# Kernel tuning notes

Hardware: AMD Instinct MI355X
Metric: run time of the kernel (lower is better)

## Reference

```python
import jax, jax.numpy as jnp
import numpy as np

B, N, D = 8, 4096, 512

def setup_inputs() -> dict:
    key = jax.random.key(0)
    k1, k2, k3 = jax.random.split(key, 3)
    x = jax.random.normal(k1, (B, N, D), dtype=jnp.float32)
    rotation = jax.random.normal(k2, (D, D), dtype=jnp.float32)
    entangle = jax.random.normal(k3, (D, D), dtype=jnp.float32)
    return {"x": x, "rotation": rotation, "entangle": entangle}

def reference(x, rotation, entangle):
    # query/key projections; note: no V projection, V = x
    query = jnp.einsum("bnd,de->bne", x, rotation)
    key = jnp.einsum("bnd,de->bne", x, entangle)
    scale = 1.0 / jnp.sqrt(jnp.asarray(x.shape[-1], dtype=x.dtype))
    scores = jax.nn.softmax(jnp.einsum("bqd,bkd->bqk", query, key) * scale, axis=-1)
    return jnp.einsum("bqk,bkd->bqd", scores, x)
```

## Files before the change

kernel.cpp:

```cpp
#include <hip/hip_runtime.h>

#define BATCH 8
#define SEQ   4096
#define DIM   512

typedef __attribute__((ext_vector_type(8))) short bf16x8;
typedef __attribute__((ext_vector_type(4))) float f32x4;

__device__ __forceinline__ unsigned short f2bf(float f) {
  unsigned int u = __float_as_uint(f);
  unsigned int r = (u + 0x7fffu + ((u >> 16) & 1u)) >> 16;
  return (unsigned short)r;
}
__device__ __forceinline__ float bf2f(unsigned short s) {
  return __uint_as_float(((unsigned int)s) << 16);
}

__global__ __launch_bounds__(256) void wt_split_kernel(
    const float* __restrict__ rot, const float* __restrict__ ent,
    unsigned short* __restrict__ wrh, unsigned short* __restrict__ wrl,
    unsigned short* __restrict__ weh, unsigned short* __restrict__ wel) {
  const float scale = 0.04419417382415922f;
  int g = blockIdx.x * 256 + threadIdx.x;
  for (int idx = g; idx < 512 * 512; idx += 128 * 256) {
    int d = idx >> 9, e = idx & 511;
    size_t o = (size_t)e * 512 + d;
    float v = rot[idx] * scale;
    unsigned short h = f2bf(v);
    wrh[o] = h; wrl[o] = f2bf(v - bf2f(h));
    float v2 = ent[idx];
    unsigned short h2 = f2bf(v2);
    weh[o] = h2; wel[o] = f2bf(v2 - bf2f(h2));
  }
}

__global__ __launch_bounds__(256) void xt_split_kernel(
    const float* __restrict__ X, unsigned short* __restrict__ Th) {
  __shared__ float T[64][65];
  const int b = blockIdx.z, n0 = blockIdx.x * 64, d0 = blockIdx.y * 64;
  const int tid = threadIdx.x;
  for (int idx = tid; idx < 4096; idx += 256) {
    int r = idx >> 6, c = idx & 63;
    T[r][c] = X[((size_t)(b * SEQ + n0 + r)) * DIM + d0 + c];
  }
  __syncthreads();
  for (int idx = tid; idx < 4096; idx += 256) {
    int r = idx >> 6, c = idx & 63;
    size_t o = ((size_t)(b * DIM + d0 + r)) * SEQ + n0 + c;
    Th[o] = f2bf(T[c][r]);
  }
}

__global__ __launch_bounds__(256, 2) void proj_both(
    const float* __restrict__ X,
    const unsigned short* __restrict__ wrh, const unsigned short* __restrict__ wrl,
    const unsigned short* __restrict__ weh, const unsigned short* __restrict__ wel,
    unsigned short* __restrict__ qh, unsigned short* __restrict__ ql,
    unsigned short* __restrict__ kh, unsigned short* __restrict__ kl) {
  const int tid = threadIdx.x;
  const int w = tid >> 6, lane = tid & 63, l15 = lane & 15, quad = lane >> 4;
  const int rowBase = blockIdx.y * 64 + (w & 1) * 32;
  const int colBase = blockIdx.x * 64 + (w >> 1) * 32;
  f32x4 qa[2][2] = {}, ka[2][2] = {};
  const float* xp[2];
  const unsigned short *rh[2], *rl[2], *eh[2], *el[2];
  xp[0] = X + (size_t)(rowBase + l15) * DIM + quad * 8;
  xp[1] = X + (size_t)(rowBase + 16 + l15) * DIM + quad * 8;
#pragma unroll
  for (int ni = 0; ni < 2; ++ni) {
    size_t o = (size_t)(colBase + ni * 16 + l15) * DIM + quad * 8;
    rh[ni] = wrh + o; rl[ni] = wrl + o; eh[ni] = weh + o; el[ni] = wel + o;
  }
  for (int d0 = 0; d0 < DIM; d0 += 32) {
    bf16x8 ah[2], al[2];
#pragma unroll
    for (int mi = 0; mi < 2; ++mi) {
      const float* p = xp[mi] + d0;
#pragma unroll
      for (int e = 0; e < 8; ++e) {
        float v = p[e];
        unsigned short h = f2bf(v);
        ah[mi][e] = (short)h;
        al[mi][e] = (short)f2bf(v - bf2f(h));
      }
    }
#pragma unroll
    for (int ni = 0; ni < 2; ++ni) {
      bf16x8 bh = *(const bf16x8*)(rh[ni] + d0);
      bf16x8 bl = *(const bf16x8*)(rl[ni] + d0);
      bf16x8 ch = *(const bf16x8*)(eh[ni] + d0);
      bf16x8 cl = *(const bf16x8*)(el[ni] + d0);
#pragma unroll
      for (int mi = 0; mi < 2; ++mi) {
        qa[mi][ni] = __builtin_amdgcn_mfma_f32_16x16x32_bf16(ah[mi], bh, qa[mi][ni], 0, 0, 0);
        qa[mi][ni] = __builtin_amdgcn_mfma_f32_16x16x32_bf16(ah[mi], bl, qa[mi][ni], 0, 0, 0);
        qa[mi][ni] = __builtin_amdgcn_mfma_f32_16x16x32_bf16(al[mi], bh, qa[mi][ni], 0, 0, 0);
        ka[mi][ni] = __builtin_amdgcn_mfma_f32_16x16x32_bf16(ah[mi], ch, ka[mi][ni], 0, 0, 0);
        ka[mi][ni] = __builtin_amdgcn_mfma_f32_16x16x32_bf16(ah[mi], cl, ka[mi][ni], 0, 0, 0);
        ka[mi][ni] = __builtin_amdgcn_mfma_f32_16x16x32_bf16(al[mi], ch, ka[mi][ni], 0, 0, 0);
      }
    }
  }
#pragma unroll
  for (int mi = 0; mi < 2; ++mi)
#pragma unroll
    for (int ni = 0; ni < 2; ++ni)
#pragma unroll
      for (int r = 0; r < 4; ++r) {
        int row = rowBase + mi * 16 + quad * 4 + r;
        int col = colBase + ni * 16 + l15;
        size_t o = (size_t)row * DIM + col;
        float v = qa[mi][ni][r];
        unsigned short h = f2bf(v);
        qh[o] = h; ql[o] = f2bf(v - bf2f(h));
        float v2 = ka[mi][ni][r];
        unsigned short h2 = f2bf(v2);
        kh[o] = h2; kl[o] = f2bf(v2 - bf2f(h2));
      }
}

__global__ __launch_bounds__(256, 2) void attn_mfma(
    const unsigned short* __restrict__ Qh, const unsigned short* __restrict__ Ql,
    const unsigned short* __restrict__ Kh, const unsigned short* __restrict__ Kl,
    const unsigned short* __restrict__ Xth, float* __restrict__ out,
    float* __restrict__ Opart, float* __restrict__ Mp, float* __restrict__ Lp) {
  __shared__ short stage[2][4][2048];
  __shared__ unsigned short PsH[64][72];
  __shared__ float red1[64][2], red2[64][2];
  __shared__ float m_s[64], l_s[64], al_s[64];

  const int tid = threadIdx.x;
  const int w = tid >> 6, lane = tid & 63, l15 = lane & 15, quad = lane >> 4;
  const int b = blockIdx.y, q0 = blockIdx.x * 64;
  const int qsp = (w & 1) * 2, ksp = (w >> 1) * 2;
  const int dbase = w * 128;
  const int ktiles = (SEQ / 64) / gridDim.z;
  const int kbase = blockIdx.z * ktiles * 64;

  if (tid < 64) { m_s[tid] = -3.0e38f; l_s[tid] = 0.0f; }
  __syncthreads();

  f32x4 Of[4][8] = {};

  const int sr = lane >> 2, scm = lane & 3;
  const unsigned short* qsrc = ((w & 1) ? Ql : Qh) + (size_t)(b * SEQ + q0) * DIM;
  const unsigned short* ksrcb = ((w & 1) ? Kl : Kh) + (size_t)b * SEQ * DIM;
  const bool isQ = (w < 2);

  for (int t = 0; t < ktiles; ++t) {
    const int k0 = kbase + t * 64;
    const unsigned short* base = isQ ? qsrc : (ksrcb + (size_t)k0 * DIM);

    {
      bf16x8 g[4];
#pragma unroll
      for (int i = 0; i < 4; ++i) {
        int r = i * 16 + sr, clog = scm ^ (r & 3);
        g[i] = *(const bf16x8*)(base + (size_t)r * DIM + clog * 8);
      }
#pragma unroll
      for (int i = 0; i < 4; ++i) {
        int r = i * 16 + sr;
        *(bf16x8*)&stage[0][w][r * 32 + scm * 8] = g[i];
      }
    }
    __syncthreads();

    f32x4 sa[2][2] = {};
    for (int c = 0; c < 16; ++c) {
      const int bsel = c & 1;
      bf16x8 g[4];
      if (c < 15) {
        const int d0 = (c + 1) * 32;
#pragma unroll
        for (int i = 0; i < 4; ++i) {
          int r = i * 16 + sr, clog = scm ^ (r & 3);
          g[i] = *(const bf16x8*)(base + (size_t)r * DIM + d0 + clog * 8);
        }
      }
      const int cq = (quad ^ (l15 & 3)) * 8;
      bf16x8 a0h = *(const bf16x8*)&stage[bsel][0][((qsp + 0) * 16 + l15) * 32 + cq];
      bf16x8 a0l = *(const bf16x8*)&stage[bsel][1][((qsp + 0) * 16 + l15) * 32 + cq];
      bf16x8 a1h = *(const bf16x8*)&stage[bsel][0][((qsp + 1) * 16 + l15) * 32 + cq];
      bf16x8 a1l = *(const bf16x8*)&stage[bsel][1][((qsp + 1) * 16 + l15) * 32 + cq];
      bf16x8 b0h = *(const bf16x8*)&stage[bsel][2][((ksp + 0) * 16 + l15) * 32 + cq];
      bf16x8 b0l = *(const bf16x8*)&stage[bsel][3][((ksp + 0) * 16 + l15) * 32 + cq];
      bf16x8 b1h = *(const bf16x8*)&stage[bsel][2][((ksp + 1) * 16 + l15) * 32 + cq];
      bf16x8 b1l = *(const bf16x8*)&stage[bsel][3][((ksp + 1) * 16 + l15) * 32 + cq];
      sa[0][0] = __builtin_amdgcn_mfma_f32_16x16x32_bf16(a0h, b0h, sa[0][0], 0, 0, 0);
      sa[0][0] = __builtin_amdgcn_mfma_f32_16x16x32_bf16(a0h, b0l, sa[0][0], 0, 0, 0);
      sa[0][0] = __builtin_amdgcn_mfma_f32_16x16x32_bf16(a0l, b0h, sa[0][0], 0, 0, 0);
      sa[0][1] = __builtin_amdgcn_mfma_f32_16x16x32_bf16(a0h, b1h, sa[0][1], 0, 0, 0);
      sa[0][1] = __builtin_amdgcn_mfma_f32_16x16x32_bf16(a0h, b1l, sa[0][1], 0, 0, 0);
      sa[0][1] = __builtin_amdgcn_mfma_f32_16x16x32_bf16(a0l, b1h, sa[0][1], 0, 0, 0);
      sa[1][0] = __builtin_amdgcn_mfma_f32_16x16x32_bf16(a1h, b0h, sa[1][0], 0, 0, 0);
      sa[1][0] = __builtin_amdgcn_mfma_f32_16x16x32_bf16(a1h, b0l, sa[1][0], 0, 0, 0);
      sa[1][0] = __builtin_amdgcn_mfma_f32_16x16x32_bf16(a1l, b0h, sa[1][0], 0, 0, 0);
      sa[1][1] = __builtin_amdgcn_mfma_f32_16x16x32_bf16(a1h, b1h, sa[1][1], 0, 0, 0);
      sa[1][1] = __builtin_amdgcn_mfma_f32_16x16x32_bf16(a1h, b1l, sa[1][1], 0, 0, 0);
      sa[1][1] = __builtin_amdgcn_mfma_f32_16x16x32_bf16(a1l, b1h, sa[1][1], 0, 0, 0);
      if (c < 15) {
#pragma unroll
        for (int i = 0; i < 4; ++i) {
          int r = i * 16 + sr;
          *(bf16x8*)&stage[1 - bsel][w][r * 32 + scm * 8] = g[i];
        }
      }
      __syncthreads();
    }

    float pm[2][4];
#pragma unroll
    for (int qi = 0; qi < 2; ++qi)
#pragma unroll
      for (int r = 0; r < 4; ++r) {
        float v = fmaxf(sa[qi][0][r], sa[qi][1][r]);
#pragma unroll
        for (int off = 1; off < 16; off <<= 1)
          v = fmaxf(v, __shfl_xor(v, off, 64));
        pm[qi][r] = v;
      }
    if (l15 == 0) {
#pragma unroll
      for (int qi = 0; qi < 2; ++qi)
#pragma unroll
        for (int r = 0; r < 4; ++r)
          red1[(qsp + qi) * 16 + quad * 4 + r][w >> 1] = pm[qi][r];
    }
    __syncthreads();
    if (tid < 64) {
      float mo = m_s[tid];
      float mn = fmaxf(mo, fmaxf(red1[tid][0], red1[tid][1]));
      m_s[tid] = mn;
      al_s[tid] = __expf(mo - mn);
    }
    __syncthreads();

#pragma unroll
    for (int qi = 0; qi < 2; ++qi)
#pragma unroll
      for (int r = 0; r < 4; ++r) {
        const int row = (qsp + qi) * 16 + quad * 4 + r;
        const float m = m_s[row];
        float p0 = __expf(sa[qi][0][r] - m);
        float p1 = __expf(sa[qi][1][r] - m);
        PsH[row][ksp * 16 + l15] = f2bf(p0);
        PsH[row][ksp * 16 + 16 + l15] = f2bf(p1);
        float v = p0 + p1;
#pragma unroll
        for (int off = 1; off < 16; off <<= 1)
          v += __shfl_xor(v, off, 64);
        if (l15 == 0) red2[row][w >> 1] = v;
      }
    __syncthreads();
    if (tid < 64) l_s[tid] = l_s[tid] * al_s[tid] + red2[tid][0] + red2[tid][1];

    float alv[4][4];
#pragma unroll
    for (int qt = 0; qt < 4; ++qt)
#pragma unroll
      for (int r = 0; r < 4; ++r)
        alv[qt][r] = al_s[qt * 16 + quad * 4 + r];
#pragma unroll
    for (int qt = 0; qt < 4; ++qt)
#pragma unroll
      for (int nt = 0; nt < 8; ++nt)
#pragma unroll
        for (int r = 0; r < 4; ++r)
          Of[qt][nt][r] *= alv[qt][r];
#pragma unroll
    for (int ks = 0; ks < 2; ++ks) {
      bf16x8 Ph[4];
#pragma unroll
      for (int qt = 0; qt < 4; ++qt)
        Ph[qt] = *(const bf16x8*)&PsH[qt * 16 + l15][ks * 32 + quad * 8];
      bf16x8 xf[8];
#pragma unroll
      for (int nt = 0; nt < 8; ++nt) {
        const size_t xo =
            ((size_t)(b * DIM + dbase + nt * 16 + l15)) * SEQ + k0 + ks * 32 + quad * 8;
        xf[nt] = *(const bf16x8*)(Xth + xo);
      }
#pragma unroll
      for (int nt = 0; nt < 8; ++nt)
#pragma unroll
        for (int qt = 0; qt < 4; ++qt)
          Of[qt][nt] = __builtin_amdgcn_mfma_f32_16x16x32_bf16(Ph[qt], xf[nt], Of[qt][nt], 0, 0, 0);
    }
    __syncthreads();
  }

  if (gridDim.z == 1) {
    float inv[4][4];
#pragma unroll
    for (int qt = 0; qt < 4; ++qt)
#pragma unroll
      for (int r = 0; r < 4; ++r)
        inv[qt][r] = 1.0f / l_s[qt * 16 + quad * 4 + r];
#pragma unroll
    for (int qt = 0; qt < 4; ++qt)
#pragma unroll
      for (int r = 0; r < 4; ++r) {
        const size_t ro = ((size_t)(b * SEQ + q0 + qt * 16 + quad * 4 + r)) * DIM + dbase;
#pragma unroll
        for (int nt = 0; nt < 8; ++nt)
          out[ro + nt * 16 + l15] = Of[qt][nt][r] * inv[qt][r];
      }
  } else {
    const size_t NE = (size_t)BATCH * SEQ * DIM;
    float* Ob = Opart + (size_t)blockIdx.z * NE;
#pragma unroll
    for (int qt = 0; qt < 4; ++qt)
#pragma unroll
      for (int r = 0; r < 4; ++r) {
        const size_t ro = ((size_t)(b * SEQ + q0 + qt * 16 + quad * 4 + r)) * DIM + dbase;
#pragma unroll
        for (int nt = 0; nt < 8; ++nt)
          Ob[ro + nt * 16 + l15] = Of[qt][nt][r];
      }
    if (tid < 64) {
      size_t ri = (size_t)blockIdx.z * (BATCH * SEQ) + (size_t)b * SEQ + q0 + tid;
      Mp[ri] = m_s[tid];
      Lp[ri] = l_s[tid];
    }
  }
}

__global__ __launch_bounds__(256) void merge_kernel(
    const float* __restrict__ Op, const float* __restrict__ Mp,
    const float* __restrict__ Lp, float* __restrict__ out) {
  const size_t NE = (size_t)BATCH * SEQ * DIM;
  const int NR = BATCH * SEQ;
  size_t i4 = (size_t)blockIdx.x * 256 + threadIdx.x;
  size_t e = i4 * 4;
  int row = (int)(e >> 9);
  float m0 = Mp[row], m1 = Mp[NR + row];
  float l0 = Lp[row], l1 = Lp[NR + row];
  float m = fmaxf(m0, m1);
  float a0 = __expf(m0 - m), a1 = __expf(m1 - m);
  float inv = 1.0f / (a0 * l0 + a1 * l1);
  float4 o0 = *(const float4*)(Op + e);
  float4 o1 = *(const float4*)(Op + NE + e);
  float4 r;
  r.x = (a0 * o0.x + a1 * o1.x) * inv;
  r.y = (a0 * o0.y + a1 * o1.y) * inv;
  r.z = (a0 * o0.z + a1 * o1.z) * inv;
  r.w = (a0 * o0.w + a1 * o1.w) * inv;
  *(float4*)(out + e) = r;
}

extern "C" void kernel_launch(void* const* d_in, const int* in_sizes, int n_in,
                              void* d_out, int out_size, void* d_ws,
                              size_t ws_size, hipStream_t stream) {
  const float* x   = (const float*)d_in[0];
  const float* rot = (const float*)d_in[1];
  const float* ent = (const float*)d_in[2];
  float* out = (float*)d_out;

  const size_t NE = (size_t)BATCH * SEQ * DIM;
  unsigned short* qh  = (unsigned short*)d_ws;
  unsigned short* ql  = qh + NE;
  unsigned short* kh  = ql + NE;
  unsigned short* kl  = kh + NE;
  unsigned short* xth = kl + NE;
  unsigned short* wrh = xth + NE;
  unsigned short* wrl = wrh + 262144;
  unsigned short* weh = wrl + 262144;
  unsigned short* wel = weh + 262144;
  float* Opart = (float*)(wel + 262144);
  float* Mp    = Opart + 2 * NE;
  float* Lp    = Mp + 2 * (BATCH * SEQ);

  const size_t need2 =
      (5 * NE + 4 * 262144) * sizeof(unsigned short) +
      (2 * NE + 4 * (size_t)(BATCH * SEQ)) * sizeof(float);
  const int splits = (ws_size >= need2) ? 2 : 1;

  wt_split_kernel<<<128, 256, 0, stream>>>(rot, ent, wrh, wrl, weh, wel);
  xt_split_kernel<<<dim3(SEQ / 64, DIM / 64, BATCH), 256, 0, stream>>>(x, xth);
  proj_both<<<dim3(DIM / 64, BATCH * SEQ / 64), 256, 0, stream>>>(
      x, wrh, wrl, weh, wel, qh, ql, kh, kl);

  attn_mfma<<<dim3(SEQ / 64, BATCH, splits), 256, 0, stream>>>(
      qh, ql, kh, kl, xth, out, Opart, Mp, Lp);
  if (splits == 2) {
    merge_kernel<<<(unsigned)(NE / 1024), 256, 0, stream>>>(Opart, Mp, Lp, out);
  }
}
```

Before: 1.573 ms.

## Pre-split x to bf16 hi/lo and enlarge attention tile to 128 queries

A new kernel splits x into bf16 high/low planes once, so the projection kernel loads them directly instead of converting fp32 per tile. The attention kernel now uses 512-thread blocks covering 128 query rows, with each wave owning 64 output columns. Each K tile and X^T fragment is therefore reused across twice as many queries, and the redundant trailing sync per tile is dropped. The cost is more registers and LDS per block and half as many blocks. The x split buffers reuse the Opart workspace before attention overwrites it.

```diff
diff --git a/kernel.cpp b/kernel.cpp
--- a/kernel.cpp
+++ b/kernel.cpp
@@ -6,6 +6,7 @@
 
 typedef __attribute__((ext_vector_type(8))) short bf16x8;
 typedef __attribute__((ext_vector_type(4))) float f32x4;
+typedef __attribute__((ext_vector_type(4))) unsigned short us16x4;
 
 __device__ __forceinline__ unsigned short f2bf(float f) {
   unsigned int u = __float_as_uint(f);
@@ -34,6 +35,23 @@
   }
 }
 
+__global__ __launch_bounds__(256) void x_split_kernel(
+    const float* __restrict__ X, unsigned short* __restrict__ Xh,
+    unsigned short* __restrict__ Xl) {
+  size_t i = ((size_t)blockIdx.x * 256 + threadIdx.x) * 4;
+  float4 v = *(const float4*)(X + i);
+  us16x4 hh, ll;
+  float vv[4] = {v.x, v.y, v.z, v.w};
+#pragma unroll
+  for (int e = 0; e < 4; ++e) {
+    unsigned short h = f2bf(vv[e]);
+    hh[e] = h;
+    ll[e] = f2bf(vv[e] - bf2f(h));
+  }
+  *(us16x4*)(Xh + i) = hh;
+  *(us16x4*)(Xl + i) = ll;
+}
+
 __global__ __launch_bounds__(256) void xt_split_kernel(
     const float* __restrict__ X, unsigned short* __restrict__ Th) {
   __shared__ float T[64][65];
@@ -52,7 +70,7 @@
 }
 
 __global__ __launch_bounds__(256, 2) void proj_both(
-    const float* __restrict__ X,
+    const unsigned short* __restrict__ Xh, const unsigned short* __restrict__ Xl,
     const unsigned short* __restrict__ wrh, const unsigned short* __restrict__ wrl,
     const unsigned short* __restrict__ weh, const unsigned short* __restrict__ wel,
     unsigned short* __restrict__ qh, unsigned short* __restrict__ ql,
@@ -62,10 +80,10 @@
   const int rowBase = blockIdx.y * 64 + (w & 1) * 32;
   const int colBase = blockIdx.x * 64 + (w >> 1) * 32;
   f32x4 qa[2][2] = {}, ka[2][2] = {};
-  const float* xp[2];
+  size_t xo[2];
   const unsigned short *rh[2], *rl[2], *eh[2], *el[2];
-  xp[0] = X + (size_t)(rowBase + l15) * DIM + quad * 8;
-  xp[1] = X + (size_t)(rowBase + 16 + l15) * DIM + quad * 8;
+  xo[0] = (size_t)(rowBase + l15) * DIM + quad * 8;
+  xo[1] = (size_t)(rowBase + 16 + l15) * DIM + quad * 8;
 #pragma unroll
   for (int ni = 0; ni < 2; ++ni) {
     size_t o = (size_t)(colBase + ni * 16 + l15) * DIM + quad * 8;
@@ -75,14 +93,8 @@
     bf16x8 ah[2], al[2];
 #pragma unroll
     for (int mi = 0; mi < 2; ++mi) {
-      const float* p = xp[mi] + d0;
-#pragma unroll
-      for (int e = 0; e < 8; ++e) {
-        float v = p[e];
-        unsigned short h = f2bf(v);
-        ah[mi][e] = (short)h;
-        al[mi][e] = (short)f2bf(v - bf2f(h));
-      }
+      ah[mi] = *(const bf16x8*)(Xh + xo[mi] + d0);
+      al[mi] = *(const bf16x8*)(Xl + xo[mi] + d0);
     }
 #pragma unroll
     for (int ni = 0; ni < 2; ++ni) {
@@ -119,74 +131,72 @@
       }
 }
 
-__global__ __launch_bounds__(256, 2) void attn_mfma(
+__global__ __launch_bounds__(512, 4) void attn_mfma(
     const unsigned short* __restrict__ Qh, const unsigned short* __restrict__ Ql,
     const unsigned short* __restrict__ Kh, const unsigned short* __restrict__ Kl,
     const unsigned short* __restrict__ Xth, float* __restrict__ out,
     float* __restrict__ Opart, float* __restrict__ Mp, float* __restrict__ Lp) {
-  __shared__ short stage[2][4][2048];
-  __shared__ unsigned short PsH[64][72];
-  __shared__ float red1[64][2], red2[64][2];
-  __shared__ float m_s[64], l_s[64], al_s[64];
+  __shared__ short stage[2][12288];
+  __shared__ unsigned short PsH[128][72];
+  __shared__ float red1[128][2], red2[128][2];
+  __shared__ float m_s[128], l_s[128], al_s[128];
 
   const int tid = threadIdx.x;
   const int w = tid >> 6, lane = tid & 63, l15 = lane & 15, quad = lane >> 4;
-  const int b = blockIdx.y, q0 = blockIdx.x * 64;
-  const int qsp = (w & 1) * 2, ksp = (w >> 1) * 2;
-  const int dbase = w * 128;
+  const int b = blockIdx.y, q0 = blockIdx.x * 128;
+  const int qsp = (w & 3) * 2, ksp = (w >> 2) * 2;
   const int ktiles = (SEQ / 64) / gridDim.z;
   const int kbase = blockIdx.z * ktiles * 64;
 
-  if (tid < 64) { m_s[tid] = -3.0e38f; l_s[tid] = 0.0f; }
+  if (tid < 128) { m_s[tid] = -3.0e38f; l_s[tid] = 0.0f; }
   __syncthreads();
 
-  f32x4 Of[4][8] = {};
+  f32x4 Of[8][4] = {};
 
   const int sr = lane >> 2, scm = lane & 3;
-  const unsigned short* qsrc = ((w & 1) ? Ql : Qh) + (size_t)(b * SEQ + q0) * DIM;
-  const unsigned short* ksrcb = ((w & 1) ? Kl : Kh) + (size_t)b * SEQ * DIM;
-  const bool isQ = (w < 2);
+  const int jblk = scm ^ ((sr >> 1) & 3);
+  const bool isQ = (w < 4);
+  const int rbase = isQ ? (w & 1) * 64 : ((w >> 1) & 1) * 32;
+  const int ninst = isQ ? 4 : 2;
+  const int plane_off = isQ ? ((w >> 1) & 1) * 4096 : 8192 + (w & 1) * 2048;
+  const unsigned short* gQ = (((w >> 1) & 1) ? Ql : Qh) + (size_t)(b * SEQ + q0) * DIM;
+  const unsigned short* gK = ((w & 1) ? Kl : Kh) + (size_t)b * SEQ * DIM;
+  const int pb = (quad ^ ((l15 >> 1) & 3)) * 8;
 
   for (int t = 0; t < ktiles; ++t) {
     const int k0 = kbase + t * 64;
-    const unsigned short* base = isQ ? qsrc : (ksrcb + (size_t)k0 * DIM);
-
-    {
-      bf16x8 g[4];
-#pragma unroll
-      for (int i = 0; i < 4; ++i) {
-        int r = i * 16 + sr, clog = scm ^ (r & 3);
-        g[i] = *(const bf16x8*)(base + (size_t)r * DIM + clog * 8);
-      }
-#pragma unroll
-      for (int i = 0; i < 4; ++i) {
-        int r = i * 16 + sr;
-        *(bf16x8*)&stage[0][w][r * 32 + scm * 8] = g[i];
-      }
-    }
+    const unsigned short* gbase = isQ ? gQ : (gK + (size_t)k0 * DIM);
+
+    bf16x8 g[4];
+#pragma unroll
+    for (int i = 0; i < 4; ++i)
+      if (i < ninst)
+        g[i] = *(const bf16x8*)(gbase + (size_t)(rbase + i * 16 + sr) * DIM + jblk * 8);
+#pragma unroll
+    for (int i = 0; i < 4; ++i)
+      if (i < ninst)
+        *(bf16x8*)&stage[0][plane_off + (rbase + i * 16 + sr) * 32 + scm * 8] = g[i];
     __syncthreads();
 
     f32x4 sa[2][2] = {};
     for (int c = 0; c < 16; ++c) {
       const int bsel = c & 1;
-      bf16x8 g[4];
       if (c < 15) {
         const int d0 = (c + 1) * 32;
 #pragma unroll
-        for (int i = 0; i < 4; ++i) {
-          int r = i * 16 + sr, clog = scm ^ (r & 3);
-          g[i] = *(const bf16x8*)(base + (size_t)r * DIM + d0 + clog * 8);
-        }
-      }
-      const int cq = (quad ^ (l15 & 3)) * 8;
-      bf16x8 a0h = *(const bf16x8*)&stage[bsel][0][((qsp + 0) * 16 + l15) * 32 + cq];
-      bf16x8 a0l = *(const bf16x8*)&stage[bsel][1][((qsp + 0) * 16 + l15) * 32 + cq];
-      bf16x8 a1h = *(const bf16x8*)&stage[bsel][0][((qsp + 1) * 16 + l15) * 32 + cq];
-      bf16x8 a1l = *(const bf16x8*)&stage[bsel][1][((qsp + 1) * 16 + l15) * 32 + cq];
-      bf16x8 b0h = *(const bf16x8*)&stage[bsel][2][((ksp + 0) * 16 + l15) * 32 + cq];
-      bf16x8 b0l = *(const bf16x8*)&stage[bsel][3][((ksp + 0) * 16 + l15) * 32 + cq];
-      bf16x8 b1h = *(const bf16x8*)&stage[bsel][2][((ksp + 1) * 16 + l15) * 32 + cq];
-      bf16x8 b1l = *(const bf16x8*)&stage[bsel][3][((ksp + 1) * 16 + l15) * 32 + cq];
+        for (int i = 0; i < 4; ++i)
+          if (i < ninst)
+            g[i] = *(const bf16x8*)(gbase + (size_t)(rbase + i * 16 + sr) * DIM + d0 + jblk * 8);
+      }
+      const short* st = stage[bsel];
+      bf16x8 a0h = *(const bf16x8*)&st[((qsp + 0) * 16 + l15) * 32 + pb];
+      bf16x8 a1h = *(const bf16x8*)&st[((qsp + 1) * 16 + l15) * 32 + pb];
+      bf16x8 a0l = *(const bf16x8*)&st[4096 + ((qsp + 0) * 16 + l15) * 32 + pb];
+      bf16x8 a1l = *(const bf16x8*)&st[4096 + ((qsp + 1) * 16 + l15) * 32 + pb];
+      bf16x8 b0h = *(const bf16x8*)&st[8192 + ((ksp + 0) * 16 + l15) * 32 + pb];
+      bf16x8 b1h = *(const bf16x8*)&st[8192 + ((ksp + 1) * 16 + l15) * 32 + pb];
+      bf16x8 b0l = *(const bf16x8*)&st[10240 + ((ksp + 0) * 16 + l15) * 32 + pb];
+      bf16x8 b1l = *(const bf16x8*)&st[10240 + ((ksp + 1) * 16 + l15) * 32 + pb];
       sa[0][0] = __builtin_amdgcn_mfma_f32_16x16x32_bf16(a0h, b0h, sa[0][0], 0, 0, 0);
       sa[0][0] = __builtin_amdgcn_mfma_f32_16x16x32_bf16(a0h, b0l, sa[0][0], 0, 0, 0);
       sa[0][0] = __builtin_amdgcn_mfma_f32_16x16x32_bf16(a0l, b0h, sa[0][0], 0, 0, 0);
@@ -201,10 +211,9 @@
       sa[1][1] = __builtin_amdgcn_mfma_f32_16x16x32_bf16(a1l, b1h, sa[1][1], 0, 0, 0);
       if (c < 15) {
 #pragma unroll
-        for (int i = 0; i < 4; ++i) {
-          int r = i * 16 + sr;
-          *(bf16x8*)&stage[1 - bsel][w][r * 32 + scm * 8] = g[i];
-        }
+        for (int i = 0; i < 4; ++i)
+          if (i < ninst)
+            *(bf16x8*)&stage[1 - bsel][plane_off + (rbase + i * 16 + sr) * 32 + scm * 8] = g[i];
       }
       __syncthreads();
     }
@@ -225,10 +234,10 @@
       for (int qi = 0; qi < 2; ++qi)
 #pragma unroll
         for (int r = 0; r < 4; ++r)
-          red1[(qsp + qi) * 16 + quad * 4 + r][w >> 1] = pm[qi][r];
+          red1[(qsp + qi) * 16 + quad * 4 + r][w >> 2] = pm[qi][r];
     }
     __syncthreads();
-    if (tid < 64) {
+    if (tid < 128) {
       float mo = m_s[tid];
       float mn = fmaxf(mo, fmaxf(red1[tid][0], red1[tid][1]));
       m_s[tid] = mn;
@@ -245,80 +254,75 @@
         float p0 = __expf(sa[qi][0][r] - m);
         float p1 = __expf(sa[qi][1][r] - m);
         PsH[row][ksp * 16 + l15] = f2bf(p0);
-        PsH[row][ksp * 16 + 16 + l15] = f2bf(p1);
+        PsH[row][(ksp + 1) * 16 + l15] = f2bf(p1);
         float v = p0 + p1;
 #pragma unroll
         for (int off = 1; off < 16; off <<= 1)
           v += __shfl_xor(v, off, 64);
-        if (l15 == 0) red2[row][w >> 1] = v;
+        if (l15 == 0) red2[row][w >> 2] = v;
       }
     __syncthreads();
-    if (tid < 64) l_s[tid] = l_s[tid] * al_s[tid] + red2[tid][0] + red2[tid][1];
-
-    float alv[4][4];
-#pragma unroll
-    for (int qt = 0; qt < 4; ++qt)
+    if (tid < 128) l_s[tid] = l_s[tid] * al_s[tid] + red2[tid][0] + red2[tid][1];
+
+    float alv[8][4];
+#pragma unroll
+    for (int qt = 0; qt < 8; ++qt)
 #pragma unroll
       for (int r = 0; r < 4; ++r)
         alv[qt][r] = al_s[qt * 16 + quad * 4 + r];
 #pragma unroll
-    for (int qt = 0; qt < 4; ++qt)
-#pragma unroll
-      for (int nt = 0; nt < 8; ++nt)
+    for (int qt = 0; qt < 8; ++qt)
+#pragma unroll
+      for (int nt = 0; nt < 4; ++nt)
 #pragma unroll
         for (int r = 0; r < 4; ++r)
           Of[qt][nt][r] *= alv[qt][r];
 #pragma unroll
     for (int ks = 0; ks < 2; ++ks) {
-      bf16x8 Ph[4];
-#pragma unroll
-      for (int qt = 0; qt < 4; ++qt)
+      bf16x8 Ph[8];
+#pragma unroll
+      for (int qt = 0; qt < 8; ++qt)
         Ph[qt] = *(const bf16x8*)&PsH[qt * 16 + l15][ks * 32 + quad * 8];
-      bf16x8 xf[8];
-#pragma unroll
-      for (int nt = 0; nt < 8; ++nt) {
+      bf16x8 xf[4];
+#pragma unroll
+      for (int nt = 0; nt < 4; ++nt) {
         const size_t xo =
-            ((size_t)(b * DIM + dbase + nt * 16 + l15)) * SEQ + k0 + ks * 32 + quad * 8;
+            ((size_t)(b * DIM + w * 64 + nt * 16 + l15)) * SEQ + k0 + ks * 32 + quad * 8;
         xf[nt] = *(const bf16x8*)(Xth + xo);
       }
 #pragma unroll
-      for (int nt = 0; nt < 8; ++nt)
-#pragma unroll
-        for (int qt = 0; qt < 4; ++qt)
+      for (int nt = 0; nt < 4; ++nt)
+#pragma unroll
+        for (int qt = 0; qt < 8; ++qt)
           Of[qt][nt] = __builtin_amdgcn_mfma_f32_16x16x32_bf16(Ph[qt], xf[nt], Of[qt][nt], 0, 0, 0);
     }
-    __syncthreads();
-  }
-
+  }
+
+  __syncthreads();
   if (gridDim.z == 1) {
-    float inv[4][4];
-#pragma unroll
-    for (int qt = 0; qt < 4; ++qt)
-#pragma unroll
-      for (int r = 0; r < 4; ++r)
-        inv[qt][r] = 1.0f / l_s[qt * 16 + quad * 4 + r];
-#pragma unroll
-    for (int qt = 0; qt < 4; ++qt)
-#pragma unroll
-      for (int r = 0; r < 4; ++r) {
-        const size_t ro = ((size_t)(b * SEQ + q0 + qt * 16 + quad * 4 + r)) * DIM + dbase;
-#pragma unroll
-        for (int nt = 0; nt < 8; ++nt)
-          out[ro + nt * 16 + l15] = Of[qt][nt][r] * inv[qt][r];
+#pragma unroll
+    for (int qt = 0; qt < 8; ++qt)
+#pragma unroll
+      for (int r = 0; r < 4; ++r) {
+        const float inv = 1.0f / l_s[qt * 16 + quad * 4 + r];
+        const size_t ro = ((size_t)(b * SEQ + q0 + qt * 16 + quad * 4 + r)) * DIM + w * 64;
+#pragma unroll
+        for (int nt = 0; nt < 4; ++nt)
+          out[ro + nt * 16 + l15] = Of[qt][nt][r] * inv;
       }
   } else {
     const size_t NE = (size_t)BATCH * SEQ * DIM;
     float* Ob = Opart + (size_t)blockIdx.z * NE;
 #pragma unroll
-    for (int qt = 0; qt < 4; ++qt)
-#pragma unroll
-      for (int r = 0; r < 4; ++r) {
-        const size_t ro = ((size_t)(b * SEQ + q0 + qt * 16 + quad * 4 + r)) * DIM + dbase;
-#pragma unroll
-        for (int nt = 0; nt < 8; ++nt)
+    for (int qt = 0; qt < 8; ++qt)
+#pragma unroll
+      for (int r = 0; r < 4; ++r) {
+        const size_t ro = ((size_t)(b * SEQ + q0 + qt * 16 + quad * 4 + r)) * DIM + w * 64;
+#pragma unroll
+        for (int nt = 0; nt < 4; ++nt)
           Ob[ro + nt * 16 + l15] = Of[qt][nt][r];
       }
-    if (tid < 64) {
+    if (tid < 128) {
       size_t ri = (size_t)blockIdx.z * (BATCH * SEQ) + (size_t)b * SEQ + q0 + tid;
       Mp[ri] = m_s[tid];
       Lp[ri] = l_s[tid];
@@ -370,6 +374,8 @@
   float* Opart = (float*)(wel + 262144);
   float* Mp    = Opart + 2 * NE;
   float* Lp    = Mp + 2 * (BATCH * SEQ);
+  unsigned short* xh = (unsigned short*)Opart;
+  unsigned short* xl = xh + NE;
 
   const size_t need2 =
       (5 * NE + 4 * 262144) * sizeof(unsigned short) +
@@ -377,11 +383,12 @@
   const int splits = (ws_size >= need2) ? 2 : 1;
 
   wt_split_kernel<<<128, 256, 0, stream>>>(rot, ent, wrh, wrl, weh, wel);
+  x_split_kernel<<<(unsigned)(NE / 1024), 256, 0, stream>>>(x, xh, xl);
   xt_split_kernel<<<dim3(SEQ / 64, DIM / 64, BATCH), 256, 0, stream>>>(x, xth);
   proj_both<<<dim3(DIM / 64, BATCH * SEQ / 64), 256, 0, stream>>>(
-      x, wrh, wrl, weh, wel, qh, ql, kh, kl);
-
-  attn_mfma<<<dim3(SEQ / 64, BATCH, splits), 256, 0, stream>>>(
+      xh, xl, wrh, wrl, weh, wel, qh, ql, kh, kl);
+
+  attn_mfma<<<dim3(SEQ / 128, BATCH, splits), 512, 0, stream>>>(
       qh, ql, kh, kl, xth, out, Opart, Mp, Lp);
   if (splits == 2) {
     merge_kernel<<<(unsigned)(NE / 1024), 256, 0, stream>>>(Opart, Mp, Lp, out);
```

New measurement: 4.612 ms. 2.93x slower.
